# Kernel tuning notes

Measured on AMD Instinct MI355X. Metric: run time of the kernel, lower is better.

Reference implementation:

```python
import jax, jax.numpy as jnp
import numpy as np

B, S, D, F, E, R = 16, 1024, 1024, 4096, 8, 32
LORA_ALPHA = 16
SCALING = LORA_ALPHA / R  # 0.5


def setup_inputs() -> dict:
    key = jax.random.key(0)
    ks = jax.random.split(key, 16)
    sd = 0.02
    return {
        "x": jax.random.normal(ks[0], (B, S, D), jnp.float32),
        "router_w": jax.random.normal(ks[1], (E, D), jnp.float32) * sd,
        "router_b": jnp.zeros((E,), jnp.float32),
        "fc1_w": jax.random.normal(ks[2], (F, D), jnp.float32) * sd,
        "fc1_b": jnp.zeros((F,), jnp.float32),
        "fc2_w": jax.random.normal(ks[3], (D, F), jnp.float32) * sd,
        "fc2_b": jnp.zeros((D,), jnp.float32),
        "down_A_w": jax.random.normal(ks[4], (E, R, D), jnp.float32) * sd,
        "down_A_b": jnp.zeros((E, R), jnp.float32),
        "down_B_w": jax.random.normal(ks[5], (E, F, R), jnp.float32) * sd,
        "down_B_b": jnp.zeros((E, F), jnp.float32),
        "up_A_w": jax.random.normal(ks[6], (E, R, F), jnp.float32) * sd,
        "up_A_b": jnp.zeros((E, R), jnp.float32),
        "up_B_w": jax.random.normal(ks[7], (E, D, R), jnp.float32) * sd,
        "up_B_b": jnp.zeros((E, D), jnp.float32),
    }


def _lora_moe_sparse(inp, onehot, A_w, A_b, B_w, B_b):
    # inp: [b,t,c_in]; onehot: [b,t,E] hard top-1 dispatch mask
    # h: per-expert rank activations [b,t,E,R] (small: R=32)
    h = jnp.einsum('btc,erc->bter', inp, A_w) + A_b
    g = h * onehot[..., None]  # zero out non-selected experts (sparse dispatch)
    out = jnp.einsum('bter,eor->bto', g, B_w)
    out = out + jnp.einsum('bte,eo->bto', onehot, B_b)
    return out * SCALING


def reference(x, router_w, router_b, fc1_w, fc1_b, fc2_w, fc2_b,
              down_A_w, down_A_b, down_B_w, down_B_b,
              up_A_w, up_A_b, up_B_w, up_B_b):
    # router + top-1 hard routing (straight-through expert_choice)
    logits = jnp.einsum('btd,ed->bte', x, router_w) + router_b
    routing = jax.nn.softmax(logits, axis=-1)
    idx = jnp.argmax(routing, axis=-1)                       # [b,t]
    y_hard = jax.nn.one_hot(idx, E, dtype=x.dtype)           # [b,t,E]
    expert_choice = y_hard - jax.lax.stop_gradient(routing) + routing

    # down proj: frozen fc1 + sparse LoRA combine (dropout p=0.05 -> eval/identity)
    h1 = jnp.einsum('btd,fd->btf', x, fc1_w) + fc1_b
    h1 = h1 + _lora_moe_sparse(x, y_hard, down_A_w, down_A_b, down_B_w, down_B_b)
    a = jax.nn.gelu(h1, approximate=False)

    # up proj: frozen fc2 + sparse LoRA combine
    out = jnp.einsum('btf,df->btd', a, fc2_w) + fc2_b
    out = out + _lora_moe_sparse(a, y_hard, up_A_w, up_A_b, up_B_w, up_B_b)
    return out, (routing, expert_choice)
```

## Files before the change

kernel.cpp:

```cpp
#include <hip/hip_runtime.h>
#include <hip/hip_bf16.h>
#include <math.h>


#define M_TOK 16384
#define DIM_D 1024
#define DIM_F 4096
#define NEXP 8
#define RANK 32
#define NER 256

typedef __attribute__((ext_vector_type(8))) short bf16x8;
typedef __attribute__((ext_vector_type(4))) float f32x4;

__device__ inline short f2bs(float x) {
  __hip_bfloat16 h = __float2bfloat16(x);
  return *reinterpret_cast<short*>(&h);
}

__device__ inline void async16(const void* g, void* l) {
  __builtin_amdgcn_global_load_lds(
      (__attribute__((address_space(1))) void*)(g),
      (__attribute__((address_space(3))) void*)(l), 16, 0, 0);
}

__global__ __launch_bounds__(256) void convert_bf16(
    const float* __restrict__ in, short* __restrict__ out, int n8)
{
  const int i = blockIdx.x * 256 + threadIdx.x;
  if (i >= n8) return;
  const float4* p = (const float4*)in + 2 * (size_t)i;
  float4 u = p[0], v = p[1];
  bf16x8 r;
  r[0] = f2bs(u.x); r[1] = f2bs(u.y); r[2] = f2bs(u.z); r[3] = f2bs(u.w);
  r[4] = f2bs(v.x); r[5] = f2bs(v.y); r[6] = f2bs(v.z); r[7] = f2bs(v.w);
  *(bf16x8*)(out + 8 * (size_t)i) = r;
}

__global__ __launch_bounds__(256) void router_kernel(
    const float* __restrict__ X,
    const float* __restrict__ RW,
    const float* __restrict__ RB,
    float* __restrict__ routing_out,
    float* __restrict__ ec_out,
    int* __restrict__ idx_out)
{
  const int wave = threadIdx.x >> 6;
  const int lane = threadIdx.x & 63;
  const int t = blockIdx.x * 4 + wave;

  const float4* xp = (const float4*)(X + (size_t)t * DIM_D);
  float4 xv[4];
#pragma unroll
  for (int i = 0; i < 4; ++i) xv[i] = xp[lane + 64 * i];

  float logit[NEXP];
#pragma unroll
  for (int e = 0; e < NEXP; ++e) {
    const float4* wp = (const float4*)(RW + (size_t)e * DIM_D);
    double p = 0.0;
#pragma unroll
    for (int i = 0; i < 4; ++i) {
      float4 w = wp[lane + 64 * i];
      p += (double)xv[i].x * w.x + (double)xv[i].y * w.y +
           (double)xv[i].z * w.z + (double)xv[i].w * w.w;
    }
#pragma unroll
    for (int off = 32; off > 0; off >>= 1) p += __shfl_xor(p, off);
    logit[e] = (float)p + RB[e];
  }
  float m = logit[0];
  int am = 0;
#pragma unroll
  for (int e = 1; e < NEXP; ++e)
    if (logit[e] > m) { m = logit[e]; am = e; }
  float pr[NEXP], s = 0.f;
#pragma unroll
  for (int e = 0; e < NEXP; ++e) { pr[e] = expf(logit[e] - m); s += pr[e]; }
  const float inv = 1.f / s;
  if (lane < NEXP) {
    float r = pr[lane] * inv;
    routing_out[(size_t)t * NEXP + lane] = r;
    float y = (lane == am) ? 1.f : 0.f;
    ec_out[(size_t)t * NEXP + lane] = (y - r) + r;
  }
  if (lane == 0) idx_out[t] = am;
}

template <int KMAIN, int DO_LORA, int EPI>
__global__ __launch_bounds__(256, 2) void gemm_bf16(
    const short* __restrict__ A, const short* __restrict__ Bm,
    const short* __restrict__ G2, const short* __restrict__ LW,
    const float* __restrict__ LB, const float* __restrict__ bias,
    const int* __restrict__ idx, void* __restrict__ outv, int N)
{
  __shared__ __align__(16) short As[128 * 32];
  __shared__ __align__(16) short Bs[128 * 32];

  const int tid = threadIdx.x;
  const int m0 = blockIdx.y * 128;
  const int n0 = blockIdx.x * 128;
  const int lane = tid & 63;
  const int wv = tid >> 6;
  const int quad = lane >> 4;
  const int lrow = lane & 15;
  const int wr = wv >> 1;
  const int wc = wv & 1;
  const int r0 = tid >> 2;
  const int c4 = (tid & 3) * 8;

  f32x4 acc[4][4];
#pragma unroll
  for (int i = 0; i < 4; ++i)
#pragma unroll
    for (int j = 0; j < 4; ++j) acc[i][j] = (f32x4){0.f, 0.f, 0.f, 0.f};

  constexpr int IT_MAIN = KMAIN / 32;
  constexpr int IT_TOT = IT_MAIN + (DO_LORA ? NEXP : 0);
  for (int it = 0; it < IT_TOT; ++it) {
    const short *a0, *a1, *b0, *b1;
    if (!DO_LORA || it < IT_MAIN) {
      const int k = it * 32;
      a0 = A + (size_t)(m0 + r0) * KMAIN + k + c4;
      a1 = a0 + (size_t)64 * KMAIN;
      b0 = Bm + (size_t)(n0 + r0) * KMAIN + k + c4;
      b1 = b0 + (size_t)64 * KMAIN;
    } else {
      const int e = it - IT_MAIN;
      a0 = G2 + (size_t)(m0 + r0) * NER + e * RANK + c4;
      a1 = a0 + 64 * NER;
      b0 = LW + ((size_t)e * N + n0 + r0) * RANK + c4;
      b1 = b0 + 64 * RANK;
    }
    async16(a0, &As[tid * 8]);
    async16(a1, &As[2048 + tid * 8]);
    async16(b0, &Bs[tid * 8]);
    async16(b1, &Bs[2048 + tid * 8]);
    __syncthreads();

    bf16x8 af[4], bfv[4];
#pragma unroll
    for (int i = 0; i < 4; ++i)
      af[i] = *(const bf16x8*)&As[(wr * 64 + i * 16 + lrow) * 32 + quad * 8];
#pragma unroll
    for (int j = 0; j < 4; ++j)
      bfv[j] = *(const bf16x8*)&Bs[(wc * 64 + j * 16 + lrow) * 32 + quad * 8];
#pragma unroll
    for (int i = 0; i < 4; ++i)
#pragma unroll
      for (int j = 0; j < 4; ++j)
        acc[i][j] = __builtin_amdgcn_mfma_f32_16x16x32_bf16(af[i], bfv[j],
                                                            acc[i][j], 0, 0, 0);
    __syncthreads();
  }

  float cb[4];
#pragma unroll
  for (int j = 0; j < 4; ++j) cb[j] = bias[n0 + wc * 64 + j * 16 + lrow];

#pragma unroll
  for (int i = 0; i < 4; ++i) {
#pragma unroll
    for (int reg = 0; reg < 4; ++reg) {
      const int t = m0 + wr * 64 + i * 16 + quad * 4 + reg;
      const int e = idx[t];
#pragma unroll
      for (int j = 0; j < 4; ++j) {
        const int gc = n0 + wc * 64 + j * 16 + lrow;
        float v = acc[i][j][reg];
        if (EPI == 2) {
          v = ((gc >> 5) == e) ? 0.5f * (v + cb[j]) : 0.f;
          ((short*)outv)[(size_t)t * N + gc] = f2bs(v);
        } else {
          v += cb[j] + 0.5f * LB[(size_t)e * N + gc];
          if (EPI == 1) {
            v = 0.5f * v * (1.0f + erff(v * 0.70710678118654752f));
            ((short*)outv)[(size_t)t * N + gc] = f2bs(v);
          } else {
            ((float*)outv)[(size_t)t * N + gc] = v;
          }
        }
      }
    }
  }
}

extern "C" void kernel_launch(void* const* d_in, const int* in_sizes, int n_in,
                              void* d_out, int out_size, void* d_ws, size_t ws_size,
                              hipStream_t stream) {
  (void)in_sizes; (void)n_in; (void)out_size; (void)ws_size;
  const float* x        = (const float*)d_in[0];
  const float* router_w = (const float*)d_in[1];
  const float* router_b = (const float*)d_in[2];
  const float* fc1_w    = (const float*)d_in[3];
  const float* fc1_b    = (const float*)d_in[4];
  const float* fc2_w    = (const float*)d_in[5];
  const float* fc2_b    = (const float*)d_in[6];
  const float* down_A_w = (const float*)d_in[7];
  const float* down_A_b = (const float*)d_in[8];
  const float* down_B_w = (const float*)d_in[9];
  const float* down_B_b = (const float*)d_in[10];
  const float* up_A_w   = (const float*)d_in[11];
  const float* up_A_b   = (const float*)d_in[12];
  const float* up_B_w   = (const float*)d_in[13];
  const float* up_B_b   = (const float*)d_in[14];

  char* ws = (char*)d_ws;
  size_t off = 0;
  int* idxp = (int*)ws;                    off += (size_t)M_TOK * 4;
  short* g2d  = (short*)(ws + off);        off += (size_t)M_TOK * NER * 2;
  short* g2u  = (short*)(ws + off);        off += (size_t)M_TOK * NER * 2;
  short* a_ws = (short*)(ws + off);        off += (size_t)M_TOK * DIM_F * 2;
  short* xb   = (short*)(ws + off);        off += (size_t)M_TOK * DIM_D * 2;
  short* fc1b = (short*)(ws + off);        off += (size_t)DIM_F * DIM_D * 2;
  short* fc2b = (short*)(ws + off);        off += (size_t)DIM_D * DIM_F * 2;
  short* dAb  = (short*)(ws + off);        off += (size_t)NER * DIM_D * 2;
  short* uAb  = (short*)(ws + off);        off += (size_t)NER * DIM_F * 2;
  short* dBb  = (short*)(ws + off);        off += (size_t)NEXP * DIM_F * RANK * 2;
  short* uBb  = (short*)(ws + off);        off += (size_t)NEXP * DIM_D * RANK * 2;

  float* out = (float*)d_out;
  float* routing = out + (size_t)M_TOK * DIM_D;
  float* ec = routing + (size_t)M_TOK * NEXP;

  auto conv = [&](const float* src, short* dst, size_t n) {
    int n8 = (int)(n / 8);
    convert_bf16<<<(n8 + 255) / 256, 256, 0, stream>>>(src, dst, n8);
  };
  conv(x, xb, (size_t)M_TOK * DIM_D);
  conv(fc1_w, fc1b, (size_t)DIM_F * DIM_D);
  conv(fc2_w, fc2b, (size_t)DIM_D * DIM_F);
  conv(down_A_w, dAb, (size_t)NER * DIM_D);
  conv(up_A_w, uAb, (size_t)NER * DIM_F);
  conv(down_B_w, dBb, (size_t)NEXP * DIM_F * RANK);
  conv(up_B_w, uBb, (size_t)NEXP * DIM_D * RANK);

  router_kernel<<<M_TOK / 4, 256, 0, stream>>>(x, router_w, router_b, routing,
                                               ec, idxp);
  gemm_bf16<DIM_D, 0, 2><<<dim3(NER / 128, M_TOK / 128), 256, 0, stream>>>(
      xb, dAb, nullptr, nullptr, nullptr, down_A_b, idxp, g2d, NER);
  gemm_bf16<DIM_D, 1, 1><<<dim3(DIM_F / 128, M_TOK / 128), 256, 0, stream>>>(
      xb, fc1b, g2d, dBb, down_B_b, fc1_b, idxp, a_ws, DIM_F);
  gemm_bf16<DIM_F, 0, 2><<<dim3(NER / 128, M_TOK / 128), 256, 0, stream>>>(
      a_ws, uAb, nullptr, nullptr, nullptr, up_A_b, idxp, g2u, NER);
  gemm_bf16<DIM_F, 1, 0><<<dim3(DIM_D / 128, M_TOK / 128), 256, 0, stream>>>(
      a_ws, fc2b, g2u, uBb, up_B_b, fc2_b, idxp, out, DIM_D);
}
```

Before: 767.6 us.

## Fuse x conversion into router, batch weight conversions, retile LoRA-A GEMMs

```diff
diff --git a/kernel.cpp b/kernel.cpp
--- a/kernel.cpp
+++ b/kernel.cpp
@@ -11,6 +11,7 @@
 #define NER 256
 
 typedef __attribute__((ext_vector_type(8))) short bf16x8;
+typedef __attribute__((ext_vector_type(4))) short bf16x4;
 typedef __attribute__((ext_vector_type(4))) float f32x4;
 
 __device__ inline short f2bs(float x) {
@@ -24,17 +25,26 @@
       (__attribute__((address_space(3))) void*)(l), 16, 0, 0);
 }
 
-__global__ __launch_bounds__(256) void convert_bf16(
-    const float* __restrict__ in, short* __restrict__ out, int n8)
-{
+struct Conv6 {
+  const float* src[6];
+  short* dst[6];
+  int base[6];
+  int total;
+};
+
+__global__ __launch_bounds__(256) void convert6(Conv6 c) {
   const int i = blockIdx.x * 256 + threadIdx.x;
-  if (i >= n8) return;
-  const float4* p = (const float4*)in + 2 * (size_t)i;
+  if (i >= c.total) return;
+  int r = 0;
+#pragma unroll
+  for (int k = 1; k < 6; ++k) r += (i >= c.base[k]);
+  const int j = i - c.base[r];
+  const float4* p = (const float4*)c.src[r] + 2 * (size_t)j;
   float4 u = p[0], v = p[1];
-  bf16x8 r;
-  r[0] = f2bs(u.x); r[1] = f2bs(u.y); r[2] = f2bs(u.z); r[3] = f2bs(u.w);
-  r[4] = f2bs(v.x); r[5] = f2bs(v.y); r[6] = f2bs(v.z); r[7] = f2bs(v.w);
-  *(bf16x8*)(out + 8 * (size_t)i) = r;
+  bf16x8 o;
+  o[0] = f2bs(u.x); o[1] = f2bs(u.y); o[2] = f2bs(u.z); o[3] = f2bs(u.w);
+  o[4] = f2bs(v.x); o[5] = f2bs(v.y); o[6] = f2bs(v.z); o[7] = f2bs(v.w);
+  *(bf16x8*)(c.dst[r] + 8 * (size_t)j) = o;
 }
 
 __global__ __launch_bounds__(256) void router_kernel(
@@ -43,7 +53,8 @@
     const float* __restrict__ RB,
     float* __restrict__ routing_out,
     float* __restrict__ ec_out,
-    int* __restrict__ idx_out)
+    int* __restrict__ idx_out,
+    short* __restrict__ xb)
 {
   const int wave = threadIdx.x >> 6;
   const int lane = threadIdx.x & 63;
@@ -53,6 +64,14 @@
   float4 xv[4];
 #pragma unroll
   for (int i = 0; i < 4; ++i) xv[i] = xp[lane + 64 * i];
+
+#pragma unroll
+  for (int i = 0; i < 4; ++i) {
+    bf16x4 o;
+    o[0] = f2bs(xv[i].x); o[1] = f2bs(xv[i].y);
+    o[2] = f2bs(xv[i].z); o[3] = f2bs(xv[i].w);
+    *(bf16x4*)(xb + (size_t)t * DIM_D + 4 * (lane + 64 * i)) = o;
+  }
 
   float logit[NEXP];
 #pragma unroll
@@ -87,7 +106,7 @@
   if (lane == 0) idx_out[t] = am;
 }
 
-template <int KMAIN, int DO_LORA, int EPI>
+template <int KMAIN, int EPI>
 __global__ __launch_bounds__(256, 2) void gemm_bf16(
     const short* __restrict__ A, const short* __restrict__ Bm,
     const short* __restrict__ G2, const short* __restrict__ LW,
@@ -115,27 +134,15 @@
 #pragma unroll
     for (int j = 0; j < 4; ++j) acc[i][j] = (f32x4){0.f, 0.f, 0.f, 0.f};
 
-  constexpr int IT_MAIN = KMAIN / 32;
-  constexpr int IT_TOT = IT_MAIN + (DO_LORA ? NEXP : 0);
-  for (int it = 0; it < IT_TOT; ++it) {
-    const short *a0, *a1, *b0, *b1;
-    if (!DO_LORA || it < IT_MAIN) {
-      const int k = it * 32;
-      a0 = A + (size_t)(m0 + r0) * KMAIN + k + c4;
-      a1 = a0 + (size_t)64 * KMAIN;
-      b0 = Bm + (size_t)(n0 + r0) * KMAIN + k + c4;
-      b1 = b0 + (size_t)64 * KMAIN;
-    } else {
-      const int e = it - IT_MAIN;
-      a0 = G2 + (size_t)(m0 + r0) * NER + e * RANK + c4;
-      a1 = a0 + 64 * NER;
-      b0 = LW + ((size_t)e * N + n0 + r0) * RANK + c4;
-      b1 = b0 + 64 * RANK;
-    }
-    async16(a0, &As[tid * 8]);
-    async16(a1, &As[2048 + tid * 8]);
-    async16(b0, &Bs[tid * 8]);
-    async16(b1, &Bs[2048 + tid * 8]);
+  const short* ap = A + (size_t)(m0 + r0) * KMAIN + c4;
+  const short* bp = Bm + (size_t)(n0 + r0) * KMAIN + c4;
+  for (int it = 0; it < KMAIN / 32; ++it) {
+    async16(ap, &As[tid * 8]);
+    async16(ap + (size_t)64 * KMAIN, &As[2048 + tid * 8]);
+    async16(bp, &Bs[tid * 8]);
+    async16(bp + (size_t)64 * KMAIN, &Bs[2048 + tid * 8]);
+    ap += 32;
+    bp += 32;
     __syncthreads();
 
     bf16x8 af[4], bfv[4];
@@ -154,6 +161,35 @@
     __syncthreads();
   }
 
+  {
+    const short* gp = G2 + (size_t)(m0 + r0) * NER + c4;
+    const short* lp = LW + (size_t)(n0 + r0) * RANK + c4;
+    for (int e = 0; e < NEXP; ++e) {
+      async16(gp, &As[tid * 8]);
+      async16(gp + 64 * NER, &As[2048 + tid * 8]);
+      async16(lp, &Bs[tid * 8]);
+      async16(lp + 64 * RANK, &Bs[2048 + tid * 8]);
+      gp += RANK;
+      lp += (size_t)N * RANK;
+      __syncthreads();
+
+      bf16x8 af[4], bfv[4];
+#pragma unroll
+      for (int i = 0; i < 4; ++i)
+        af[i] = *(const bf16x8*)&As[(wr * 64 + i * 16 + lrow) * 32 + quad * 8];
+#pragma unroll
+      for (int j = 0; j < 4; ++j)
+        bfv[j] = *(const bf16x8*)&Bs[(wc * 64 + j * 16 + lrow) * 32 + quad * 8];
+#pragma unroll
+      for (int i = 0; i < 4; ++i)
+#pragma unroll
+        for (int j = 0; j < 4; ++j)
+          acc[i][j] = __builtin_amdgcn_mfma_f32_16x16x32_bf16(af[i], bfv[j],
+                                                              acc[i][j], 0, 0, 0);
+      __syncthreads();
+    }
+  }
+
   float cb[4];
 #pragma unroll
   for (int j = 0; j < 4; ++j) cb[j] = bias[n0 + wc * 64 + j * 16 + lrow];
@@ -167,19 +203,86 @@
 #pragma unroll
       for (int j = 0; j < 4; ++j) {
         const int gc = n0 + wc * 64 + j * 16 + lrow;
-        float v = acc[i][j][reg];
-        if (EPI == 2) {
-          v = ((gc >> 5) == e) ? 0.5f * (v + cb[j]) : 0.f;
+        float v = acc[i][j][reg] + cb[j] + 0.5f * LB[(size_t)e * N + gc];
+        if (EPI == 1) {
+          v = 0.5f * v * (1.0f + erff(v * 0.70710678118654752f));
           ((short*)outv)[(size_t)t * N + gc] = f2bs(v);
         } else {
-          v += cb[j] + 0.5f * LB[(size_t)e * N + gc];
-          if (EPI == 1) {
-            v = 0.5f * v * (1.0f + erff(v * 0.70710678118654752f));
-            ((short*)outv)[(size_t)t * N + gc] = f2bs(v);
-          } else {
-            ((float*)outv)[(size_t)t * N + gc] = v;
-          }
+          ((float*)outv)[(size_t)t * N + gc] = v;
         }
+      }
+    }
+  }
+}
+
+template <int KMAIN>
+__global__ __launch_bounds__(256, 2) void lora_a_gemm(
+    const short* __restrict__ A, const short* __restrict__ W,
+    const float* __restrict__ bias,
+    const int* __restrict__ idx, short* __restrict__ g2)
+{
+  __shared__ __align__(16) short As[128 * 32];
+  __shared__ __align__(16) short Bs[64 * 32];
+
+  const int tid = threadIdx.x;
+  const int m0 = blockIdx.y * 128;
+  const int n0 = blockIdx.x * 64;
+  const int lane = tid & 63;
+  const int wv = tid >> 6;
+  const int quad = lane >> 4;
+  const int lrow = lane & 15;
+  const int wr = wv >> 1;
+  const int wc = wv & 1;
+  const int r0 = tid >> 2;
+  const int c4 = (tid & 3) * 8;
+
+  f32x4 acc[4][2];
+#pragma unroll
+  for (int i = 0; i < 4; ++i)
+#pragma unroll
+    for (int j = 0; j < 2; ++j) acc[i][j] = (f32x4){0.f, 0.f, 0.f, 0.f};
+
+  const short* ap = A + (size_t)(m0 + r0) * KMAIN + c4;
+  const short* bp = W + (size_t)(n0 + r0) * KMAIN + c4;
+  for (int it = 0; it < KMAIN / 32; ++it) {
+    async16(ap, &As[tid * 8]);
+    async16(ap + (size_t)64 * KMAIN, &As[2048 + tid * 8]);
+    async16(bp, &Bs[tid * 8]);
+    ap += 32;
+    bp += 32;
+    __syncthreads();
+
+    bf16x8 af[4], bfv[2];
+#pragma unroll
+    for (int i = 0; i < 4; ++i)
+      af[i] = *(const bf16x8*)&As[(wr * 64 + i * 16 + lrow) * 32 + quad * 8];
+#pragma unroll
+    for (int j = 0; j < 2; ++j)
+      bfv[j] = *(const bf16x8*)&Bs[(wc * 32 + j * 16 + lrow) * 32 + quad * 8];
+#pragma unroll
+    for (int i = 0; i < 4; ++i)
+#pragma unroll
+      for (int j = 0; j < 2; ++j)
+        acc[i][j] = __builtin_amdgcn_mfma_f32_16x16x32_bf16(af[i], bfv[j],
+                                                            acc[i][j], 0, 0, 0);
+    __syncthreads();
+  }
+
+  float cb[2];
+#pragma unroll
+  for (int j = 0; j < 2; ++j) cb[j] = bias[n0 + wc * 32 + j * 16 + lrow];
+
+#pragma unroll
+  for (int i = 0; i < 4; ++i) {
+#pragma unroll
+    for (int reg = 0; reg < 4; ++reg) {
+      const int t = m0 + wr * 64 + i * 16 + quad * 4 + reg;
+      const int e = idx[t];
+#pragma unroll
+      for (int j = 0; j < 2; ++j) {
+        const int gc = n0 + wc * 32 + j * 16 + lrow;
+        float v = ((gc >> 5) == e) ? 0.5f * (acc[i][j][reg] + cb[j]) : 0.f;
+        g2[(size_t)t * NER + gc] = f2bs(v);
       }
     }
   }
@@ -223,26 +326,31 @@
   float* routing = out + (size_t)M_TOK * DIM_D;
   float* ec = routing + (size_t)M_TOK * NEXP;
 
-  auto conv = [&](const float* src, short* dst, size_t n) {
-    int n8 = (int)(n / 8);
-    convert_bf16<<<(n8 + 255) / 256, 256, 0, stream>>>(src, dst, n8);
-  };
-  conv(x, xb, (size_t)M_TOK * DIM_D);
-  conv(fc1_w, fc1b, (size_t)DIM_F * DIM_D);
-  conv(fc2_w, fc2b, (size_t)DIM_D * DIM_F);
-  conv(down_A_w, dAb, (size_t)NER * DIM_D);
-  conv(up_A_w, uAb, (size_t)NER * DIM_F);
-  conv(down_B_w, dBb, (size_t)NEXP * DIM_F * RANK);
-  conv(up_B_w, uBb, (size_t)NEXP * DIM_D * RANK);
-
   router_kernel<<<M_TOK / 4, 256, 0, stream>>>(x, router_w, router_b, routing,
-                                               ec, idxp);
-  gemm_bf16<DIM_D, 0, 2><<<dim3(NER / 128, M_TOK / 128), 256, 0, stream>>>(
-      xb, dAb, nullptr, nullptr, nullptr, down_A_b, idxp, g2d, NER);
-  gemm_bf16<DIM_D, 1, 1><<<dim3(DIM_F / 128, M_TOK / 128), 256, 0, stream>>>(
+                                               ec, idxp, xb);
+
+  Conv6 c;
+  const float* srcs[6] = {fc1_w, fc2_w, down_A_w, up_A_w, down_B_w, up_B_w};
+  short* dsts[6] = {fc1b, fc2b, dAb, uAb, dBb, uBb};
+  const size_t ns[6] = {(size_t)DIM_F * DIM_D, (size_t)DIM_D * DIM_F,
+                        (size_t)NER * DIM_D,   (size_t)NER * DIM_F,
+                        (size_t)NEXP * DIM_F * RANK, (size_t)NEXP * DIM_D * RANK};
+  int acc8 = 0;
+  for (int i = 0; i < 6; ++i) {
+    c.src[i] = srcs[i];
+    c.dst[i] = dsts[i];
+    c.base[i] = acc8;
+    acc8 += (int)(ns[i] / 8);
+  }
+  c.total = acc8;
+  convert6<<<(c.total + 255) / 256, 256, 0, stream>>>(c);
+
+  lora_a_gemm<DIM_D><<<dim3(NER / 64, M_TOK / 128), 256, 0, stream>>>(
+      xb, dAb, down_A_b, idxp, g2d);
+  gemm_bf16<DIM_D, 1><<<dim3(DIM_F / 128, M_TOK / 128), 256, 0, stream>>>(
       xb, fc1b, g2d, dBb, down_B_b, fc1_b, idxp, a_ws, DIM_F);
-  gemm_bf16<DIM_F, 0, 2><<<dim3(NER / 128, M_TOK / 128), 256, 0, stream>>>(
-      a_ws, uAb, nullptr, nullptr, nullptr, up_A_b, idxp, g2u, NER);
-  gemm_bf16<DIM_F, 1, 0><<<dim3(DIM_D / 128, M_TOK / 128), 256, 0, stream>>>(
+  lora_a_gemm<DIM_F><<<dim3(NER / 64, M_TOK / 128), 256, 0, stream>>>(
+      a_ws, uAb, up_A_b, idxp, g2u);
+  gemm_bf16<DIM_F, 0><<<dim3(DIM_D / 128, M_TOK / 128), 256, 0, stream>>>(
       a_ws, fc2b, g2u, uBb, up_B_b, fc2_b, idxp, out, DIM_D);
 }
```

Result: slower. 802.9 us (+4.6%).
